# Kernel optimization log

Hardware: AMD Instinct MI355X
Metric: run time of the kernel (lower is better)

## Reference

```python
import jax, jax.numpy as jnp
import numpy as np

FS = 30.0        # sampling rate (Hz)
HIGH_PASS = 40.0 # BPM
LOW_PASS = 250.0 # BPM


def setup_inputs() -> dict:
    key = jax.random.key(0)
    k1, k2 = jax.random.split(key)
    B, N = 1024, 16384
    outputs = jax.random.normal(k1, (B, N), dtype=jnp.float32)
    # heart rates in BPM, within (high_pass, low_pass) band so slices are non-degenerate
    targets = 45.0 + 150.0 * jax.random.uniform(k2, (B, 1), dtype=jnp.float32)
    return {"outputs": outputs, "targets": targets}


def reference(outputs, targets):
    N = outputs.shape[-1]
    F = N // 2 + 1
    pulse_band = jnp.array([HIGH_PASS / 60.0, LOW_PASS / 60.0], dtype=jnp.float32)
    f = jnp.linspace(0.0, FS / 2.0, F, dtype=jnp.float32)  # [F]
    min_idx = jnp.argmin(jnp.abs(f - pulse_band[0]))
    max_idx = jnp.argmin(jnp.abs(f - pulse_band[1]))

    outputs = outputs.reshape(-1, N)
    if targets.shape[-1] != 1:
        targets = jnp.mean(targets, axis=-1, keepdims=True)
    t_hz = targets.reshape(-1) / 60.0  # [B] target frequency in Hz

    # rfft with norm='forward' divides by N, matching torch.fft.rfft(norm='forward')
    X = jnp.fft.rfft(outputs, axis=-1, norm='forward')  # [B, F] complex
    P1 = X.real ** 2 + X.imag ** 2                       # [B, F] power spectrum

    # per-sample index of the reference (ground-truth) frequency bin
    ref_idx = jnp.argmin(jnp.abs(f[None, :] - t_hz[:, None]), axis=-1)  # [B]

    # vectorized masked reduction replacing the per-sample python loop:
    # sum over [min_idx, ref_idx-1) U [ref_idx+2, max_idx)
    j = jnp.arange(F)
    ri = ref_idx[:, None]
    mask = ((j[None, :] >= min_idx) & (j[None, :] < ri - 1)) | \
           ((j[None, :] >= ri + 2) & (j[None, :] < max_idx))
    other_sum = jnp.sum(jnp.where(mask, P1, 0.0), axis=-1)              # [B]
    denom = (max_idx - min_idx - 3).astype(jnp.float32)
    other_avrg = other_sum / denom

    pulse_freq_amp = jnp.take_along_axis(P1, ref_idx[:, None], axis=-1)[:, 0]  # [B]
    snrs = 10.0 * jnp.log10(pulse_freq_amp / other_avrg)
    return -jnp.mean(snrs)
```

## Files before the change

### kernel.cpp

```cpp
#include <hip/hip_runtime.h>
#include <math.h>

#define THREADS 512
#define MHALF 8192
#define NREAL 16384
#define MIN_IDX 364
#define MAX_IDX 2276

__device__ __forceinline__ int br13(int x) {
    return (int)(__brev((unsigned)x) >> 19);
}

__device__ __forceinline__ int PHI(int i) {
    return i ^ (((i >> 5) & 15) << 1);
}

__device__ __forceinline__ float2 cmul(float2 a, float2 b) {
    return make_float2(a.x * b.x - a.y * b.y, a.x * b.y + a.y * b.x);
}

__device__ __forceinline__ void bfly(float2& a, float2& b, float2 tw) {
    float2 t = make_float2(a.x - b.x, a.y - b.y);
    a.x += b.x; a.y += b.y;
    b = cmul(t, tw);
}

__device__ __forceinline__ void fft_block16(float2 v[16], float2 W1)
{
    constexpr float C16x[8] = {1.f,  0.92387953251128674f,  0.70710678118654757f,  0.38268343236508978f,
                               0.f, -0.38268343236508978f, -0.70710678118654757f, -0.92387953251128674f};
    constexpr float C16y[8] = {0.f, -0.38268343236508978f, -0.70710678118654757f, -0.92387953251128674f,
                              -1.f, -0.92387953251128674f, -0.70710678118654757f, -0.38268343236508978f};
    constexpr float C8x[4] = {1.f,  0.70710678118654757f,  0.f, -0.70710678118654757f};
    constexpr float C8y[4] = {0.f, -0.70710678118654757f, -1.f, -0.70710678118654757f};

    float2 W2 = cmul(W1, W1), W4 = cmul(W2, W2), W8 = cmul(W4, W4);

    #pragma unroll
    for (int m = 0; m < 8; ++m) {
        float2 tw = cmul(W1, make_float2(C16x[m], C16y[m]));
        bfly(v[m], v[m + 8], tw);
    }
    #pragma unroll
    for (int g = 0; g < 2; ++g) {
        #pragma unroll
        for (int m = 0; m < 4; ++m) {
            float2 tw = cmul(W2, make_float2(C8x[m], C8y[m]));
            bfly(v[8 * g + m], v[8 * g + m + 4], tw);
        }
    }
    float2 W4i = make_float2(W4.y, -W4.x);
    #pragma unroll
    for (int g = 0; g < 4; ++g) {
        bfly(v[4 * g + 0], v[4 * g + 2], W4);
        bfly(v[4 * g + 1], v[4 * g + 3], W4i);
    }
    #pragma unroll
    for (int g = 0; g < 8; ++g)
        bfly(v[2 * g], v[2 * g + 1], W8);
}

__global__ __launch_bounds__(THREADS, 2)
void negsnr_row_kernel(const float* __restrict__ x,
                       const float* __restrict__ targets,
                       float* __restrict__ snr_out)
{
    __shared__ float2 cf[MHALF];
    const int row  = blockIdx.x;
    const int tid  = threadIdx.x;
    const int lane = tid & 63;
    const int wave = tid >> 6;

    const float step = 15.0f / 8192.0f;
    const float t_hz = targets[row] / 60.0f;
    const float c = t_hz * (8192.0f / 15.0f);
    int kf = (int)floorf(c);
    int ri = 0; float best = 1e30f;
    #pragma unroll
    for (int d = -1; d <= 2; ++d) {
        int k = min(max(kf + d, 0), 8192);
        float dist = fabsf((float)k * step - t_hz);
        if (dist < best) { best = dist; ri = k; }
    }

    const float NTWO_PI = -6.2831853071795865f;

    const float2* xr = (const float2*)(x + (size_t)row * NREAL);
    float2 v[16];
    #pragma unroll
    for (int m = 0; m < 16; ++m) v[m] = xr[tid + 512 * m];
    {
        float s_, c_;
        __sincosf(NTWO_PI * (float)tid * (1.0f / 8192.0f), &s_, &c_);
        fft_block16(v, make_float2(c_, s_));
    }
    #pragma unroll
    for (int m = 0; m < 16; ++m) cf[PHI(tid + 512 * m)] = v[m];
    __syncthreads();

    const int low5 = tid & 31;
    const int base2 = low5 + ((tid >> 5) << 9);
    #pragma unroll
    for (int m = 0; m < 16; ++m) v[m] = cf[PHI(base2 + 32 * m)];
    {
        float s_, c_;
        __sincosf(NTWO_PI * (float)low5 * (1.0f / 512.0f), &s_, &c_);
        fft_block16(v, make_float2(c_, s_));
    }
    #pragma unroll
    for (int m = 0; m < 16; ++m) cf[PHI(base2 + 32 * m)] = v[m];
    __syncthreads();

    const int p = tid & 1;
    const int base3 = p + ((tid >> 1) << 5);
    #pragma unroll
    for (int m = 0; m < 16; ++m) v[m] = cf[PHI(base3 + 2 * m)];
    {
        float2 U = p ? make_float2(0.98078528040323044f, -0.19509032201612825f)
                     : make_float2(1.0f, 0.0f);
        fft_block16(v, U);
    }
    #pragma unroll
    for (int m = 0; m < 16; ++m) cf[PHI(base3 + 2 * m)] = v[m];
    __syncthreads();

    float other = 0.0f, pulse = 0.0f;
    bool hasp = false;
    for (int k = MIN_IDX + tid; k < MAX_IDX; k += THREADS) {
        int a = br13(k);
        int b = br13(MHALF - k);
        float4 ya = *(const float4*)&cf[PHI(a)];
        float4 yb = *(const float4*)&cf[PHI(b - 1)];
        float Zr  = ya.x + ya.z, Zi  = ya.y + ya.w;
        float Zmr = yb.x - yb.z, Zmi = yb.y - yb.w;
        float xer  = 0.5f * (Zr + Zmr), xei = 0.5f * (Zi - Zmi);
        float xor_ = 0.5f * (Zi + Zmi), xoi = -0.5f * (Zr - Zmr);
        float s_, c_;
        __sincosf(NTWO_PI * (float)k * (1.0f / 16384.0f), &s_, &c_);
        float xr_ = xer + c_ * xor_ - s_ * xoi;
        float xi_ = xei + c_ * xoi + s_ * xor_;
        float pw = xr_ * xr_ + xi_ * xi_;
        if (k < ri - 1 || k > ri + 1) other += pw;
        if (k == ri) { pulse = pw; hasp = true; }
    }
    __syncthreads();
    if (hasp) cf[8].x = pulse;
    #pragma unroll
    for (int off = 32; off; off >>= 1) other += __shfl_down(other, off);
    if (lane == 0) cf[wave].x = other;
    __syncthreads();
    if (tid == 0) {
        float tot = 0.0f;
        #pragma unroll
        for (int w = 0; w < 8; ++w) tot += cf[w].x;
        const float denom = (float)(MAX_IDX - MIN_IDX - 3);
        snr_out[row] = 10.0f * log10f(cf[8].x * denom / tot);
    }
}

__global__ void negsnr_mean_kernel(const float* __restrict__ snr,
                                   float* __restrict__ out, int n)
{
    __shared__ float sacc[4];
    const int tid = threadIdx.x;
    float acc = 0.0f;
    for (int i = tid; i < n; i += 256) acc += snr[i];
    #pragma unroll
    for (int off = 32; off; off >>= 1) acc += __shfl_down(acc, off);
    if ((tid & 63) == 0) sacc[tid >> 6] = acc;
    __syncthreads();
    if (tid == 0) {
        float t = sacc[0] + sacc[1] + sacc[2] + sacc[3];
        out[0] = -t / (float)n;
    }
}

extern "C" void kernel_launch(void* const* d_in, const int* in_sizes, int n_in,
                              void* d_out, int out_size, void* d_ws, size_t ws_size,
                              hipStream_t stream) {
    const float* outputs = (const float*)d_in[0];
    const float* targets = (const float*)d_in[1];
    const int B = in_sizes[1];
    float* snr = (float*)d_ws;

    negsnr_row_kernel<<<B, THREADS, 0, stream>>>(outputs, targets, snr);
    negsnr_mean_kernel<<<1, 256, 0, stream>>>(snr, (float*)d_out, B);
}
```

Baseline: 37.27 us.

## Restructure in-LDS FFT as four radix-8 passes over 1024 threads

Replaces the three radix-16 passes, run by 512 threads per row, with four radix-8 passes run by 1024 threads per row, and adjusts the stage strides, twiddles and reduction slots to match. The goal is to halve per-thread register use and raise the number of resident waves so that LDS and global latency are better hidden. In exchange it adds an extra LDS round trip and barrier per row, and more waves take part in each block-wide sync. The launch bound hint is raised to 8 blocks, but 64KB of LDS per block still caps how many blocks each CU can hold.

```diff
diff --git a/kernel.cpp b/kernel.cpp
--- a/kernel.cpp
+++ b/kernel.cpp
@@ -1,7 +1,7 @@
 #include <hip/hip_runtime.h>
 #include <math.h>
 
-#define THREADS 512
+#define THREADS 1024
 #define MHALF 8192
 #define NREAL 16384
 #define MIN_IDX 364
@@ -25,42 +25,22 @@
     b = cmul(t, tw);
 }
 
-__device__ __forceinline__ void fft_block16(float2 v[16], float2 W1)
+__device__ __forceinline__ void fft_block8(float2 v[8], float2 W1)
 {
-    constexpr float C16x[8] = {1.f,  0.92387953251128674f,  0.70710678118654757f,  0.38268343236508978f,
-                               0.f, -0.38268343236508978f, -0.70710678118654757f, -0.92387953251128674f};
-    constexpr float C16y[8] = {0.f, -0.38268343236508978f, -0.70710678118654757f, -0.92387953251128674f,
-                              -1.f, -0.92387953251128674f, -0.70710678118654757f, -0.38268343236508978f};
-    constexpr float C8x[4] = {1.f,  0.70710678118654757f,  0.f, -0.70710678118654757f};
-    constexpr float C8y[4] = {0.f, -0.70710678118654757f, -1.f, -0.70710678118654757f};
-
-    float2 W2 = cmul(W1, W1), W4 = cmul(W2, W2), W8 = cmul(W4, W4);
-
-    #pragma unroll
-    for (int m = 0; m < 8; ++m) {
-        float2 tw = cmul(W1, make_float2(C16x[m], C16y[m]));
-        bfly(v[m], v[m + 8], tw);
-    }
-    #pragma unroll
-    for (int g = 0; g < 2; ++g) {
-        #pragma unroll
-        for (int m = 0; m < 4; ++m) {
-            float2 tw = cmul(W2, make_float2(C8x[m], C8y[m]));
-            bfly(v[8 * g + m], v[8 * g + m + 4], tw);
-        }
-    }
-    float2 W4i = make_float2(W4.y, -W4.x);
-    #pragma unroll
-    for (int g = 0; g < 4; ++g) {
-        bfly(v[4 * g + 0], v[4 * g + 2], W4);
-        bfly(v[4 * g + 1], v[4 * g + 3], W4i);
-    }
-    #pragma unroll
-    for (int g = 0; g < 8; ++g)
-        bfly(v[2 * g], v[2 * g + 1], W8);
+    const float R2 = 0.70710678118654757f;
+    float2 W2 = cmul(W1, W1), W4 = cmul(W2, W2);
+    bfly(v[0], v[4], W1);
+    bfly(v[1], v[5], cmul(W1, make_float2(R2, -R2)));
+    bfly(v[2], v[6], make_float2(W1.y, -W1.x));
+    bfly(v[3], v[7], cmul(W1, make_float2(-R2, -R2)));
+    float2 W2i = make_float2(W2.y, -W2.x);
+    bfly(v[0], v[2], W2);  bfly(v[1], v[3], W2i);
+    bfly(v[4], v[6], W2);  bfly(v[5], v[7], W2i);
+    bfly(v[0], v[1], W4);  bfly(v[2], v[3], W4);
+    bfly(v[4], v[5], W4);  bfly(v[6], v[7], W4);
 }
 
-__global__ __launch_bounds__(THREADS, 2)
+__global__ __launch_bounds__(THREADS, 8)
 void negsnr_row_kernel(const float* __restrict__ x,
                        const float* __restrict__ targets,
                        float* __restrict__ snr_out)
@@ -73,55 +53,67 @@
 
     const float step = 15.0f / 8192.0f;
     const float t_hz = targets[row] / 60.0f;
-    const float c = t_hz * (8192.0f / 15.0f);
-    int kf = (int)floorf(c);
-    int ri = 0; float best = 1e30f;
-    #pragma unroll
-    for (int d = -1; d <= 2; ++d) {
-        int k = min(max(kf + d, 0), 8192);
-        float dist = fabsf((float)k * step - t_hz);
-        if (dist < best) { best = dist; ri = k; }
+    int ri;
+    {
+        int kf = (int)floorf(t_hz * (8192.0f / 15.0f));
+        float best = 1e30f; ri = 0;
+        #pragma unroll
+        for (int d = -1; d <= 2; ++d) {
+            int k = min(max(kf + d, 0), 8192);
+            float dist = fabsf((float)k * step - t_hz);
+            if (dist < best) { best = dist; ri = k; }
+        }
     }
 
     const float NTWO_PI = -6.2831853071795865f;
+    float2 v[8];
 
-    const float2* xr = (const float2*)(x + (size_t)row * NREAL);
-    float2 v[16];
-    #pragma unroll
-    for (int m = 0; m < 16; ++m) v[m] = xr[tid + 512 * m];
     {
+        const float2* xr = (const float2*)(x + (size_t)row * NREAL);
+        #pragma unroll
+        for (int m = 0; m < 8; ++m) v[m] = xr[tid + 1024 * m];
         float s_, c_;
         __sincosf(NTWO_PI * (float)tid * (1.0f / 8192.0f), &s_, &c_);
-        fft_block16(v, make_float2(c_, s_));
+        fft_block8(v, make_float2(c_, s_));
+        #pragma unroll
+        for (int m = 0; m < 8; ++m) cf[PHI(tid + 1024 * m)] = v[m];
     }
-    #pragma unroll
-    for (int m = 0; m < 16; ++m) cf[PHI(tid + 512 * m)] = v[m];
     __syncthreads();
 
-    const int low5 = tid & 31;
-    const int base2 = low5 + ((tid >> 5) << 9);
-    #pragma unroll
-    for (int m = 0; m < 16; ++m) v[m] = cf[PHI(base2 + 32 * m)];
     {
+        const int q = tid & 127, base = q + ((tid >> 7) << 10);
+        #pragma unroll
+        for (int m = 0; m < 8; ++m) v[m] = cf[PHI(base + 128 * m)];
         float s_, c_;
-        __sincosf(NTWO_PI * (float)low5 * (1.0f / 512.0f), &s_, &c_);
-        fft_block16(v, make_float2(c_, s_));
+        __sincosf(NTWO_PI * (float)q * (1.0f / 1024.0f), &s_, &c_);
+        fft_block8(v, make_float2(c_, s_));
+        #pragma unroll
+        for (int m = 0; m < 8; ++m) cf[PHI(base + 128 * m)] = v[m];
     }
-    #pragma unroll
-    for (int m = 0; m < 16; ++m) cf[PHI(base2 + 32 * m)] = v[m];
     __syncthreads();
 
-    const int p = tid & 1;
-    const int base3 = p + ((tid >> 1) << 5);
-    #pragma unroll
-    for (int m = 0; m < 16; ++m) v[m] = cf[PHI(base3 + 2 * m)];
     {
-        float2 U = p ? make_float2(0.98078528040323044f, -0.19509032201612825f)
+        const int q = tid & 15, base = q + ((tid >> 4) << 7);
+        #pragma unroll
+        for (int m = 0; m < 8; ++m) v[m] = cf[PHI(base + 16 * m)];
+        float s_, c_;
+        __sincosf(NTWO_PI * (float)q * (1.0f / 128.0f), &s_, &c_);
+        fft_block8(v, make_float2(c_, s_));
+        #pragma unroll
+        for (int m = 0; m < 8; ++m) cf[PHI(base + 16 * m)] = v[m];
+    }
+    __syncthreads();
+
+    {
+        const int p = tid & 1, base = p + ((tid >> 1) << 4);
+        #pragma unroll
+        for (int m = 0; m < 8; ++m) v[m] = cf[PHI(base + 2 * m)];
+        float2 U = p ? make_float2(0.92387953251128674f, -0.38268343236508978f)
                      : make_float2(1.0f, 0.0f);
-        fft_block16(v, U);
+        fft_block8(v, U);
+        #pragma unroll
+        for (int m = 0; m < 8; ++m) cf[PHI(base + 2 * m)] = v[m];
     }
-    #pragma unroll
-    for (int m = 0; m < 16; ++m) cf[PHI(base3 + 2 * m)] = v[m];
     __syncthreads();
 
     float other = 0.0f, pulse = 0.0f;
@@ -144,7 +136,7 @@
         if (k == ri) { pulse = pw; hasp = true; }
     }
     __syncthreads();
-    if (hasp) cf[8].x = pulse;
+    if (hasp) cf[16].x = pulse;
     #pragma unroll
     for (int off = 32; off; off >>= 1) other += __shfl_down(other, off);
     if (lane == 0) cf[wave].x = other;
@@ -152,9 +144,9 @@
     if (tid == 0) {
         float tot = 0.0f;
         #pragma unroll
-        for (int w = 0; w < 8; ++w) tot += cf[w].x;
+        for (int w = 0; w < 16; ++w) tot += cf[w].x;
         const float denom = (float)(MAX_IDX - MIN_IDX - 3);
-        snr_out[row] = 10.0f * log10f(cf[8].x * denom / tot);
+        snr_out[row] = 10.0f * log10f(cf[16].x * denom / tot);
     }
 }
 
```

Result: slower. 38.12 us (+2.3%).
